# Performance work log

Hardware: AMD Instinct MI355X
Metric: run time of the kernel (lower is better)

Reference implementation:

```python
import jax, jax.numpy as jnp
import numpy as np

N_NODES = 50000
N_EDGES = 800000
IN_CH = 64
HEADS = 8
OUT_CH = 8
LEAKY_ALPHA = 0.3  # Keras LeakyReLU default


def setup_inputs() -> dict:
    key = jax.random.key(0)
    k1, k2, k3, k4, k5 = jax.random.split(key, 5)
    h = jax.random.normal(k1, (N_NODES, IN_CH), dtype=jnp.float32)
    W = jax.random.normal(k2, (2 * IN_CH, HEADS * OUT_CH), dtype=jnp.float32) * 0.1
    a = jax.random.normal(k3, (1, HEADS * OUT_CH), dtype=jnp.float32) * 0.1
    src = jax.random.randint(k4, (N_EDGES,), 0, N_NODES, dtype=jnp.int32)
    tgt = jax.random.randint(k5, (N_EDGES,), 0, N_NODES, dtype=jnp.int32)
    return {"h": h, "W": W, "a": a, "src": src, "tgt": tgt}


def reference(h, W, a, src, tgt):
    # h: [N, C]; W: [2C, H*D]; a: [1, H*D]; src/tgt: [E]
    N = h.shape[0]
    hi = h[src]                                   # [E, C] gather source feats
    hj = h[tgt]                                   # [E, C] gather target feats
    hij = jnp.concatenate([hi, hj], axis=-1)      # [E, 2C]
    e = jax.nn.leaky_relu(hij @ W, negative_slope=LEAKY_ALPHA)  # [E, H*D]
    # (dropout omitted: eval mode)
    e = e * a                                     # broadcast attention vector
    e = e.reshape(-1, HEADS, OUT_CH).sum(axis=-1)  # [E, H] per-head logits
    # segment softmax over target nodes (numerically stable)
    m = jax.ops.segment_max(e, tgt, num_segments=N)   # [N, H]
    ex = jnp.exp(e - m[tgt])                          # [E, H]
    s = jax.ops.segment_sum(ex, tgt, num_segments=N)  # [N, H]
    att = ex / s[tgt]                                 # [E, H]
    # weight source features per head (in_channel == head*out_channel branch)
    msg = hi.reshape(-1, HEADS, OUT_CH) * att[:, :, None]  # [E, H, D]
    out = jax.ops.segment_sum(msg.reshape(-1, HEADS * OUT_CH), tgt, num_segments=N)
    return out  # [N, H*D]
```

## Files before the change

### kernel.cpp

```cpp
#include <hip/hip_runtime.h>
#include <hip/hip_fp16.h>
#include <math.h>

#define ALPHA 0.3f
#define MAXDEG 64
#define LOG2E 1.44269504088896f
#define UVOFF (64 * 68 + 4)
#define NSLICE 512

__device__ __forceinline__ unsigned int pack2(float u, float hv) {
    __half2 p = __floats2half2_rn(u, hv);
    unsigned int w;
    __builtin_memcpy(&w, &p, 4);
    return w;
}

__device__ __forceinline__ float2 unpack2(unsigned int w) {
    __half2 p;
    __builtin_memcpy(&p, &w, 4);
    return __half22float2(p);
}

__device__ __forceinline__ float dpp_sum8(float z) {
    int t;
    t = __builtin_amdgcn_mov_dpp(__float_as_int(z), 0xB1, 0xF, 0xF, true);
    z += __int_as_float(t);
    t = __builtin_amdgcn_mov_dpp(__float_as_int(z), 0x4E, 0xF, 0xF, true);
    z += __int_as_float(t);
    t = __builtin_amdgcn_mov_dpp(__float_as_int(z), 0x141, 0xF, 0xF, true);
    z += __int_as_float(t);
    return z;
}

__global__ __launch_bounds__(256) void k_uv(const float* __restrict__ h,
                                            const float* __restrict__ W,
                                            unsigned int* __restrict__ g,
                                            float* __restrict__ vbuf,
                                            int* __restrict__ cursor,
                                            int N, int NC) {
    __shared__ float Ws[UVOFF + 64 * 68];
    const int t = threadIdx.x;
    const int gidx = blockIdx.x * 256 + t;
    if (gidx < NC) cursor[gidx] = 0;

    for (int i = t; i < 128 * 64; i += 256) {
        const int row = i >> 6, col = i & 63;
        const int idx = (row < 64) ? (row * 68 + col) : (UVOFF + (row - 64) * 68 + col);
        Ws[idx] = W[i];
    }
    __syncthreads();

    const int nb = blockIdx.x * 64;
    const int kk = t & 15;
    const int gn = t >> 4;
    const int colbase = (kk * 8) & 63;
    const int wbase   = (kk < 8) ? 0 : UVOFF;

    int nidx[4];
#pragma unroll
    for (int i = 0; i < 4; ++i) {
        int n = nb + gn * 4 + i;
        nidx[i] = (n < N) ? n : (N - 1);
    }

    float acc[4][8];
#pragma unroll
    for (int i = 0; i < 4; ++i)
#pragma unroll
        for (int j = 0; j < 8; ++j) acc[i][j] = 0.0f;

    for (int c4 = 0; c4 < 64; c4 += 4) {
        float hh[4][4];
#pragma unroll
        for (int i = 0; i < 4; ++i) {
            const float4 tv = *(const float4*)&h[(size_t)nidx[i] * 64 + c4];
            hh[i][0] = tv.x; hh[i][1] = tv.y; hh[i][2] = tv.z; hh[i][3] = tv.w;
        }
#pragma unroll
        for (int cc = 0; cc < 4; ++cc) {
            const float* wrow = &Ws[wbase + (c4 + cc) * 68 + colbase];
            const float4 w0 = *(const float4*)(wrow);
            const float4 w1 = *(const float4*)(wrow + 4);
            const float wv[8] = {w0.x, w0.y, w0.z, w0.w, w1.x, w1.y, w1.z, w1.w};
#pragma unroll
            for (int i = 0; i < 4; ++i)
#pragma unroll
                for (int j = 0; j < 8; ++j) acc[i][j] += hh[i][cc] * wv[j];
        }
    }

#pragma unroll
    for (int i = 0; i < 4; ++i) {
        const int n = nb + gn * 4 + i;
        if (n >= N) continue;
        if (kk < 8) {
            const float4 h0 = *(const float4*)&h[(size_t)n * 64 + colbase];
            const float4 h1 = *(const float4*)&h[(size_t)n * 64 + colbase + 4];
            const float hv[8] = {h0.x, h0.y, h0.z, h0.w, h1.x, h1.y, h1.z, h1.w};
            unsigned int w[8];
#pragma unroll
            for (int j = 0; j < 8; ++j) w[j] = pack2(acc[i][j], hv[j]);
            uint4 w0 = {w[0], w[1], w[2], w[3]};
            uint4 w1 = {w[4], w[5], w[6], w[7]};
            *(uint4*)&g[(size_t)n * 64 + colbase]     = w0;
            *(uint4*)&g[(size_t)n * 64 + colbase + 4] = w1;
        } else {
            float4 o0 = {acc[i][0], acc[i][1], acc[i][2], acc[i][3]};
            float4 o1 = {acc[i][4], acc[i][5], acc[i][6], acc[i][7]};
            *(float4*)&vbuf[(size_t)n * 64 + colbase]     = o0;
            *(float4*)&vbuf[(size_t)n * 64 + colbase + 4] = o1;
        }
    }
}

__global__ __launch_bounds__(256) void k_fill(const int* __restrict__ src,
                                              const int* __restrict__ tgt,
                                              int* __restrict__ cursor,
                                              unsigned short* __restrict__ srcs,
                                              int E, int NPB) {
    const int p  = blockIdx.x & 7;
    const int sl = blockIdx.x >> 3;
    const int Q  = E >> 2;
    const int per = (Q + NSLICE - 1) / NSLICE;
    const int q0 = sl * per;
    const int q1 = min(q0 + per, Q);
    const int pbase = p * NPB;

    for (int q = q0 + (int)threadIdx.x; q < q1; q += 256) {
        const int4 t4 = ((const int4*)tgt)[q];
        const bool m0 = (t4.x & 7) == p;
        const bool m1 = (t4.y & 7) == p;
        const bool m2 = (t4.z & 7) == p;
        const bool m3 = (t4.w & 7) == p;
        if (!(m0 | m1 | m2 | m3)) continue;
        const int4 s4 = ((const int4*)src)[q];
        if (m0) { const int b = pbase + (t4.x >> 3); const int pos = atomicAdd(&cursor[b], 1); if (pos < MAXDEG) srcs[(size_t)b * MAXDEG + pos] = (unsigned short)s4.x; }
        if (m1) { const int b = pbase + (t4.y >> 3); const int pos = atomicAdd(&cursor[b], 1); if (pos < MAXDEG) srcs[(size_t)b * MAXDEG + pos] = (unsigned short)s4.y; }
        if (m2) { const int b = pbase + (t4.z >> 3); const int pos = atomicAdd(&cursor[b], 1); if (pos < MAXDEG) srcs[(size_t)b * MAXDEG + pos] = (unsigned short)s4.z; }
        if (m3) { const int b = pbase + (t4.w >> 3); const int pos = atomicAdd(&cursor[b], 1); if (pos < MAXDEG) srcs[(size_t)b * MAXDEG + pos] = (unsigned short)s4.w; }
    }
    if (sl == 0) {
        for (int i = (Q << 2) + (int)threadIdx.x; i < E; i += 256) {
            const int ti = tgt[i];
            if ((ti & 7) == p) {
                const int b = pbase + (ti >> 3);
                const int pos = atomicAdd(&cursor[b], 1);
                if (pos < MAXDEG) srcs[(size_t)b * MAXDEG + pos] = (unsigned short)src[i];
            }
        }
    }
}

__global__ __launch_bounds__(256) void k_node(const unsigned int* __restrict__ g,
                                              const float* __restrict__ vbuf,
                                              const float* __restrict__ a,
                                              const int* __restrict__ cnt,
                                              const unsigned short* __restrict__ srcs,
                                              float* __restrict__ out,
                                              int N, int NPB) {
    const int lane = threadIdx.x & 63;
    const int wv0  = (blockIdx.x * 256 + threadIdx.x) >> 6;
    const int nwv  = gridDim.x * 4;
    const float a_l = a[lane] * LOG2E;

    for (int wid = wv0; wid < N; wid += nwv) {
        const int b   = (wid & 7) * NPB + (wid >> 3);
        const float v_l = vbuf[(size_t)wid * 64 + lane];
        const int num = min(cnt[b], MAXDEG);
        const int beg = b * MAXDEG;

        float l_run = 0.0f, acc = 0.0f;

        int k = 0;
        for (; k + 8 <= num; k += 8) {
            const ushort4 sa = *(const ushort4*)(srcs + beg + k);
            const ushort4 sb = *(const ushort4*)(srcs + beg + k + 4);
            unsigned int w[8];
            w[0] = g[(size_t)sa.x * 64 + lane];
            w[1] = g[(size_t)sa.y * 64 + lane];
            w[2] = g[(size_t)sa.z * 64 + lane];
            w[3] = g[(size_t)sa.w * 64 + lane];
            w[4] = g[(size_t)sb.x * 64 + lane];
            w[5] = g[(size_t)sb.y * 64 + lane];
            w[6] = g[(size_t)sb.z * 64 + lane];
            w[7] = g[(size_t)sb.w * 64 + lane];
#pragma unroll
            for (int j = 0; j < 8; ++j) {
                const float2 f = unpack2(w[j]);
                const float q = f.x + v_l;
                float z = fmaxf(q, q * ALPHA) * a_l;
                z = dpp_sum8(z);
                const float p = __builtin_amdgcn_exp2f(z);
                l_run += p;
                acc = fmaf(f.y, p, acc);
            }
        }
        if (k + 4 <= num) {
            const ushort4 sa = *(const ushort4*)(srcs + beg + k);
            unsigned int w[4];
            w[0] = g[(size_t)sa.x * 64 + lane];
            w[1] = g[(size_t)sa.y * 64 + lane];
            w[2] = g[(size_t)sa.z * 64 + lane];
            w[3] = g[(size_t)sa.w * 64 + lane];
#pragma unroll
            for (int j = 0; j < 4; ++j) {
                const float2 f = unpack2(w[j]);
                const float q = f.x + v_l;
                float z = fmaxf(q, q * ALPHA) * a_l;
                z = dpp_sum8(z);
                const float p = __builtin_amdgcn_exp2f(z);
                l_run += p;
                acc = fmaf(f.y, p, acc);
            }
            k += 4;
        }
        for (; k < num; ++k) {
            const int s = srcs[beg + k];
            const float2 f = unpack2(g[(size_t)s * 64 + lane]);
            const float q = f.x + v_l;
            float z = fmaxf(q, q * ALPHA) * a_l;
            z = dpp_sum8(z);
            const float p = __builtin_amdgcn_exp2f(z);
            l_run += p;
            acc = fmaf(f.y, p, acc);
        }

        out[(size_t)wid * 64 + lane] = (num > 0) ? (acc / l_run) : 0.0f;
    }
}

extern "C" void kernel_launch(void* const* d_in, const int* in_sizes, int n_in,
                              void* d_out, int out_size, void* d_ws, size_t ws_size,
                              hipStream_t stream) {
    const float* h   = (const float*)d_in[0];
    const float* W   = (const float*)d_in[1];
    const float* a   = (const float*)d_in[2];
    const int*   src = (const int*)d_in[3];
    const int*   tgt = (const int*)d_in[4];
    float* out = (float*)d_out;

    const int N = in_sizes[0] / 64;
    const int E = in_sizes[3];
    const int NPB = (N + 7) / 8;
    const int NC  = NPB * 8;

    unsigned int*   g      = (unsigned int*)d_ws;
    float*          vbuf   = (float*)(g + (size_t)N * 64);
    int*            cursor = (int*)(vbuf + (size_t)N * 64);
    unsigned short* srcs   = (unsigned short*)(cursor + NC);

    k_uv<<<(N + 63) / 64, 256, 0, stream>>>(h, W, g, vbuf, cursor, N, NC);
    k_fill<<<8 * NSLICE, 256, 0, stream>>>(src, tgt, cursor, srcs, E, NPB);
    k_node<<<2048, 256, 0, stream>>>(g, vbuf, a, cursor, srcs, out, N, NPB);
}
```

Before: 100.2 us.

## Fuse node projection GEMM and CSR fill into one prep kernel

Merges the per-node projection GEMM kernel and the edge-bucketing fill kernel into a single k_prep launch. The first nuvb blocks do the GEMM and then their fill slice, while the remaining blocks only do fill. Cursor zeroing moves to a hipMemsetAsync because the fill now runs alongside the GEMM. The fill grid drops from 4096 to 2048 blocks. The aim is to overlap the compute-bound GEMM with the atomic-heavy fill and save one launch, at the cost of load imbalance between GEMM blocks and fill-only blocks.

```diff
diff --git a/kernel.cpp b/kernel.cpp
--- a/kernel.cpp
+++ b/kernel.cpp
@@ -6,7 +6,7 @@
 #define MAXDEG 64
 #define LOG2E 1.44269504088896f
 #define UVOFF (64 * 68 + 4)
-#define NSLICE 512
+#define PREP_GRID 2048
 
 __device__ __forceinline__ unsigned int pack2(float u, float hv) {
     __half2 p = __floats2half2_rn(u, hv);
@@ -32,96 +32,16 @@
     return z;
 }
 
-__global__ __launch_bounds__(256) void k_uv(const float* __restrict__ h,
-                                            const float* __restrict__ W,
-                                            unsigned int* __restrict__ g,
-                                            float* __restrict__ vbuf,
-                                            int* __restrict__ cursor,
-                                            int N, int NC) {
-    __shared__ float Ws[UVOFF + 64 * 68];
-    const int t = threadIdx.x;
-    const int gidx = blockIdx.x * 256 + t;
-    if (gidx < NC) cursor[gidx] = 0;
-
-    for (int i = t; i < 128 * 64; i += 256) {
-        const int row = i >> 6, col = i & 63;
-        const int idx = (row < 64) ? (row * 68 + col) : (UVOFF + (row - 64) * 68 + col);
-        Ws[idx] = W[i];
-    }
-    __syncthreads();
-
-    const int nb = blockIdx.x * 64;
-    const int kk = t & 15;
-    const int gn = t >> 4;
-    const int colbase = (kk * 8) & 63;
-    const int wbase   = (kk < 8) ? 0 : UVOFF;
-
-    int nidx[4];
-#pragma unroll
-    for (int i = 0; i < 4; ++i) {
-        int n = nb + gn * 4 + i;
-        nidx[i] = (n < N) ? n : (N - 1);
-    }
-
-    float acc[4][8];
-#pragma unroll
-    for (int i = 0; i < 4; ++i)
-#pragma unroll
-        for (int j = 0; j < 8; ++j) acc[i][j] = 0.0f;
-
-    for (int c4 = 0; c4 < 64; c4 += 4) {
-        float hh[4][4];
-#pragma unroll
-        for (int i = 0; i < 4; ++i) {
-            const float4 tv = *(const float4*)&h[(size_t)nidx[i] * 64 + c4];
-            hh[i][0] = tv.x; hh[i][1] = tv.y; hh[i][2] = tv.z; hh[i][3] = tv.w;
-        }
-#pragma unroll
-        for (int cc = 0; cc < 4; ++cc) {
-            const float* wrow = &Ws[wbase + (c4 + cc) * 68 + colbase];
-            const float4 w0 = *(const float4*)(wrow);
-            const float4 w1 = *(const float4*)(wrow + 4);
-            const float wv[8] = {w0.x, w0.y, w0.z, w0.w, w1.x, w1.y, w1.z, w1.w};
-#pragma unroll
-            for (int i = 0; i < 4; ++i)
-#pragma unroll
-                for (int j = 0; j < 8; ++j) acc[i][j] += hh[i][cc] * wv[j];
-        }
-    }
-
-#pragma unroll
-    for (int i = 0; i < 4; ++i) {
-        const int n = nb + gn * 4 + i;
-        if (n >= N) continue;
-        if (kk < 8) {
-            const float4 h0 = *(const float4*)&h[(size_t)n * 64 + colbase];
-            const float4 h1 = *(const float4*)&h[(size_t)n * 64 + colbase + 4];
-            const float hv[8] = {h0.x, h0.y, h0.z, h0.w, h1.x, h1.y, h1.z, h1.w};
-            unsigned int w[8];
-#pragma unroll
-            for (int j = 0; j < 8; ++j) w[j] = pack2(acc[i][j], hv[j]);
-            uint4 w0 = {w[0], w[1], w[2], w[3]};
-            uint4 w1 = {w[4], w[5], w[6], w[7]};
-            *(uint4*)&g[(size_t)n * 64 + colbase]     = w0;
-            *(uint4*)&g[(size_t)n * 64 + colbase + 4] = w1;
-        } else {
-            float4 o0 = {acc[i][0], acc[i][1], acc[i][2], acc[i][3]};
-            float4 o1 = {acc[i][4], acc[i][5], acc[i][6], acc[i][7]};
-            *(float4*)&vbuf[(size_t)n * 64 + colbase]     = o0;
-            *(float4*)&vbuf[(size_t)n * 64 + colbase + 4] = o1;
-        }
-    }
-}
-
-__global__ __launch_bounds__(256) void k_fill(const int* __restrict__ src,
-                                              const int* __restrict__ tgt,
-                                              int* __restrict__ cursor,
-                                              unsigned short* __restrict__ srcs,
-                                              int E, int NPB) {
+__device__ __forceinline__ void fill_part(const int* __restrict__ src,
+                                          const int* __restrict__ tgt,
+                                          int* __restrict__ cursor,
+                                          unsigned short* __restrict__ srcs,
+                                          int E, int NPB) {
     const int p  = blockIdx.x & 7;
     const int sl = blockIdx.x >> 3;
+    const int NS = gridDim.x >> 3;
     const int Q  = E >> 2;
-    const int per = (Q + NSLICE - 1) / NSLICE;
+    const int per = (Q + NS - 1) / NS;
     const int q0 = sl * per;
     const int q1 = min(q0 + per, Q);
     const int pbase = p * NPB;
@@ -148,6 +68,100 @@
                 if (pos < MAXDEG) srcs[(size_t)b * MAXDEG + pos] = (unsigned short)src[i];
             }
         }
+    }
+}
+
+__device__ __forceinline__ void gemm_part(const float* __restrict__ h,
+                                          const float* __restrict__ W,
+                                          unsigned int* __restrict__ g,
+                                          float* __restrict__ vbuf,
+                                          float* __restrict__ Ws, int N) {
+    const int t = threadIdx.x;
+    for (int i = t; i < 128 * 64; i += 256) {
+        const int row = i >> 6, col = i & 63;
+        const int idx = (row < 64) ? (row * 68 + col) : (UVOFF + (row - 64) * 68 + col);
+        Ws[idx] = W[i];
+    }
+    __syncthreads();
+
+    const int nb = blockIdx.x * 64;
+    const int kk = t & 15;
+    const int gn = t >> 4;
+    const int colbase = (kk * 8) & 63;
+    const int wbase   = (kk < 8) ? 0 : UVOFF;
+
+    int nidx[4];
+#pragma unroll
+    for (int i = 0; i < 4; ++i) {
+        int n = nb + gn * 4 + i;
+        nidx[i] = (n < N) ? n : (N - 1);
+    }
+
+    float acc[4][8];
+#pragma unroll
+    for (int i = 0; i < 4; ++i)
+#pragma unroll
+        for (int j = 0; j < 8; ++j) acc[i][j] = 0.0f;
+
+    for (int c4 = 0; c4 < 64; c4 += 4) {
+        float hh[4][4];
+#pragma unroll
+        for (int i = 0; i < 4; ++i) {
+            const float4 tv = *(const float4*)&h[(size_t)nidx[i] * 64 + c4];
+            hh[i][0] = tv.x; hh[i][1] = tv.y; hh[i][2] = tv.z; hh[i][3] = tv.w;
+        }
+#pragma unroll
+        for (int cc = 0; cc < 4; ++cc) {
+            const float* wrow = &Ws[wbase + (c4 + cc) * 68 + colbase];
+            const float4 w0 = *(const float4*)(wrow);
+            const float4 w1 = *(const float4*)(wrow + 4);
+            const float wv[8] = {w0.x, w0.y, w0.z, w0.w, w1.x, w1.y, w1.z, w1.w};
+#pragma unroll
+            for (int i = 0; i < 4; ++i)
+#pragma unroll
+                for (int j = 0; j < 8; ++j) acc[i][j] += hh[i][cc] * wv[j];
+        }
+    }
+
+#pragma unroll
+    for (int i = 0; i < 4; ++i) {
+        const int n = nb + gn * 4 + i;
+        if (n >= N) continue;
+        if (kk < 8) {
+            const float4 h0 = *(const float4*)&h[(size_t)n * 64 + colbase];
+            const float4 h1 = *(const float4*)&h[(size_t)n * 64 + colbase + 4];
+            const float hv[8] = {h0.x, h0.y, h0.z, h0.w, h1.x, h1.y, h1.z, h1.w};
+            unsigned int w[8];
+#pragma unroll
+            for (int j = 0; j < 8; ++j) w[j] = pack2(acc[i][j], hv[j]);
+            uint4 w0 = {w[0], w[1], w[2], w[3]};
+            uint4 w1 = {w[4], w[5], w[6], w[7]};
+            *(uint4*)&g[(size_t)n * 64 + colbase]     = w0;
+            *(uint4*)&g[(size_t)n * 64 + colbase + 4] = w1;
+        } else {
+            float4 o0 = {acc[i][0], acc[i][1], acc[i][2], acc[i][3]};
+            float4 o1 = {acc[i][4], acc[i][5], acc[i][6], acc[i][7]};
+            *(float4*)&vbuf[(size_t)n * 64 + colbase]     = o0;
+            *(float4*)&vbuf[(size_t)n * 64 + colbase + 4] = o1;
+        }
+    }
+}
+
+__global__ __launch_bounds__(256) void k_prep(const float* __restrict__ h,
+                                              const float* __restrict__ W,
+                                              const int* __restrict__ src,
+                                              const int* __restrict__ tgt,
+                                              unsigned int* __restrict__ g,
+                                              float* __restrict__ vbuf,
+                                              int* __restrict__ cursor,
+                                              unsigned short* __restrict__ srcs,
+                                              int N, int E, int NPB, int nuvb) {
+    __shared__ float Ws[UVOFF + 64 * 68];
+    if ((int)blockIdx.x < nuvb) {
+        gemm_part(h, W, g, vbuf, Ws, N);
+        fill_part(src, tgt, cursor, srcs, E, NPB);
+    } else {
+        fill_part(src, tgt, cursor, srcs, E, NPB);
     }
 }
 
@@ -243,13 +257,14 @@
     const int E = in_sizes[3];
     const int NPB = (N + 7) / 8;
     const int NC  = NPB * 8;
+    const int nuvb = (N + 63) / 64;
 
     unsigned int*   g      = (unsigned int*)d_ws;
     float*          vbuf   = (float*)(g + (size_t)N * 64);
     int*            cursor = (int*)(vbuf + (size_t)N * 64);
     unsigned short* srcs   = (unsigned short*)(cursor + NC);
 
-    k_uv<<<(N + 63) / 64, 256, 0, stream>>>(h, W, g, vbuf, cursor, N, NC);
-    k_fill<<<8 * NSLICE, 256, 0, stream>>>(src, tgt, cursor, srcs, E, NPB);
+    hipMemsetAsync(cursor, 0, (size_t)NC * sizeof(int), stream);
+    k_prep<<<PREP_GRID, 256, 0, stream>>>(h, W, src, tgt, g, vbuf, cursor, srcs, N, E, NPB, nuvb);
     k_node<<<2048, 256, 0, stream>>>(g, vbuf, a, cursor, srcs, out, N, NPB);
 }
```

Measured after the change: 95.59 us. -4.6%, faster.
